# Optimization experiments

Measured on AMD Instinct MI355X. Metric: run time of the kernel, lower is better.

Reference implementation:

```python
import jax, jax.numpy as jnp
import numpy as np

RPN_BATCH = 256
ROI_BATCH = 128
IMG = 800.0


def _box_iou(a, b):
    # a: [N,4], b: [G,4] -> [N,G]
    lt = jnp.maximum(a[:, None, :2], b[None, :, :2])
    rb = jnp.minimum(a[:, None, 2:], b[None, :, 2:])
    wh = jnp.clip(rb - lt, 0.0)
    inter = wh[..., 0] * wh[..., 1]
    area_a = (a[:, 2] - a[:, 0]) * (a[:, 3] - a[:, 1])
    area_b = (b[:, 2] - b[:, 0]) * (b[:, 3] - b[:, 1])
    return inter / (area_a[:, None] + area_b[None, :] - inter + 1e-6)


def _encode(a, t):
    wa = a[:, 2] - a[:, 0]
    ha = a[:, 3] - a[:, 1]
    xa = a[:, 0] + 0.5 * wa
    ya = a[:, 1] + 0.5 * ha
    wt = t[:, 2] - t[:, 0]
    ht = t[:, 3] - t[:, 1]
    xt = t[:, 0] + 0.5 * wt
    yt = t[:, 1] + 0.5 * ht
    return jnp.stack(((xt - xa) / wa, (yt - ya) / ha,
                      jnp.log(wt / wa + 1e-6), jnp.log(ht / ha + 1e-6)), axis=1)


def _smooth_l1(x):
    ax = jnp.abs(x)
    return jnp.where(ax < 1.0, 0.5 * x * x, ax - 0.5)


def _rpn_loss_one(scores, deltas, anchors, gt):
    # scores [N,1], deltas [N,4], anchors [N,4], gt [G,4]
    ious = _box_iou(anchors, gt)                 # [N,G]
    max_iou = ious.max(axis=1)
    argmax = ious.argmax(axis=1)
    labels = jnp.full((anchors.shape[0],), -1.0, dtype=scores.dtype)
    labels = jnp.where(max_iou < 0.3, 0.0, labels)
    labels = jnp.where(max_iou > 0.7, 1.0, labels)
    labels = labels.at[jnp.argmax(ious, axis=0)].set(1.0)  # each gt's best anchor is positive
    # deterministic subsampling: keep first K in index order (replaces randperm)
    num_pos = RPN_BATCH // 2
    pos = labels == 1.0
    labels = jnp.where(pos & (jnp.cumsum(pos) > num_pos), -1.0, labels)
    n_pos = jnp.sum(labels == 1.0)
    neg = labels == 0.0
    labels = jnp.where(neg & (jnp.cumsum(neg) > (RPN_BATCH - n_pos)), -1.0, labels)
    mask = (labels != -1.0).astype(scores.dtype)
    logit = scores[:, 0]
    t = jnp.clip(labels, 0.0, 1.0)
    bce = jnp.maximum(logit, 0.0) - logit * t + jnp.log1p(jnp.exp(-jnp.abs(logit)))
    cls = jnp.sum(bce * mask) / jnp.maximum(jnp.sum(mask), 1.0)
    tgt = _encode(anchors, gt[argmax])
    posm = (labels == 1.0).astype(scores.dtype)
    n_posf = jnp.sum(posm)
    reg = jnp.where(n_posf > 0,
                    jnp.sum(_smooth_l1(deltas - tgt) * posm[:, None])
                    / jnp.maximum(n_posf * 4.0, 1.0),
                    0.0)
    return cls + reg


def _det_loss_one(cls_scores, bbox_deltas, proposals, gt, gt_labels):
    # cls_scores [P,C], bbox_deltas [P,4C], proposals [P,4], gt [G,4], gt_labels [G]
    P = proposals.shape[0]
    ious = _box_iou(proposals, gt)
    max_iou = ious.max(axis=1)
    argmax = ious.argmax(axis=1)
    assigned = jnp.where(max_iou >= 0.5, gt_labels[argmax], 0)
    num_pos = ROI_BATCH // 4
    pos = assigned > 0
    pos_rank = jnp.cumsum(pos) - 1
    neg_rank = jnp.cumsum(~pos) - 1
    idx = jnp.arange(P)
    # sort key: first up-to-num_pos positives (index order), then negatives,
    # excess positives pushed to the end -> first ROI_BATCH entries are the sample
    key = jnp.where(pos,
                    jnp.where(pos_rank < num_pos, pos_rank, 2 * P + idx),
                    P + neg_rank)
    sampled = jnp.argsort(key)[:ROI_BATCH]
    t_labels = assigned[sampled]
    matched = gt[argmax[sampled]]
    t_deltas = _encode(proposals[sampled], matched)
    logp = jax.nn.log_softmax(cls_scores[sampled], axis=-1)
    cls = -jnp.mean(jnp.take_along_axis(logp, t_labels[:, None], axis=1)[:, 0])
    pd = bbox_deltas[sampled].reshape(ROI_BATCH, -1, 4)
    preds = pd[jnp.arange(ROI_BATCH), t_labels]  # class-specific deltas
    posm = (t_labels > 0).astype(cls_scores.dtype)
    n_pos = jnp.sum(posm)
    reg = jnp.where(n_pos > 0,
                    jnp.sum(_smooth_l1(preds - t_deltas) * posm[:, None])
                    / jnp.maximum(n_pos * 4.0, 1.0),
                    0.0)
    return cls + reg


def _rand_boxes(k, prefix):
    k1, k2 = jax.random.split(k)
    xy = jax.random.uniform(k1, prefix + (2,)) * (IMG - 130.0)
    wh = jax.random.uniform(k2, prefix + (2,)) * 120.0 + 8.0
    return jnp.concatenate([xy, xy + wh], axis=-1)


def setup_inputs() -> dict:
    B, N, P, G, C = 4, 250000, 1000, 32, 81
    key = jax.random.key(0)
    ks = jax.random.split(key, 8)
    return {
        "rpn_scores": jax.random.normal(ks[0], (B, N, 1), dtype=jnp.float32),
        "rpn_deltas": jax.random.normal(ks[1], (B, N, 4), dtype=jnp.float32) * 0.1,
        "cls_scores": jax.random.normal(ks[2], (B * P, C), dtype=jnp.float32),
        "bbox_deltas": jax.random.normal(ks[3], (B * P, 4 * C), dtype=jnp.float32) * 0.1,
        "anchors": _rand_boxes(ks[4], (N,)),
        "proposals": _rand_boxes(ks[5], (B, P)),
        "gt_boxes": _rand_boxes(ks[6], (B, G)),
        "gt_labels": jax.random.randint(ks[7], (B, G), 1, C, dtype=jnp.int32),
    }


def reference(rpn_scores, rpn_deltas, cls_scores, bbox_deltas,
              anchors, proposals, gt_boxes, gt_labels):
    B, P, _ = proposals.shape
    C = cls_scores.shape[-1]
    cls_b = cls_scores.reshape(B, P, C)
    del_b = bbox_deltas.reshape(B, P, 4 * C)
    rpn = jax.vmap(lambda s, d, g: _rpn_loss_one(s, d, anchors, g))(
        rpn_scores, rpn_deltas, gt_boxes)
    det = jax.vmap(_det_loss_one)(cls_b, del_b, proposals, gt_boxes, gt_labels)
    return jnp.sum(rpn) + jnp.sum(det)
```

## Files before the change

### kernel.cpp

```cpp
#include <hip/hip_runtime.h>
#include <math.h>
#include <stdint.h>

#define B_ 4
#define N_ 250000
#define P_ 1000
#define G_ 32
#define C_ 81
#define RPN_BATCH 256
#define ROI_BATCH 128

#define ABLK 1024
#define NBA ((N_ + ABLK - 1) / ABLK)

__device__ __forceinline__ float iou_one(float a0, float a1, float a2, float a3,
                                         float areaA,
                                         float b0, float b1, float b2, float b3) {
    float ltx = fmaxf(a0, b0), lty = fmaxf(a1, b1);
    float rbx = fminf(a2, b2), rby = fminf(a3, b3);
    float w = fmaxf(rbx - ltx, 0.f), h = fmaxf(rby - lty, 0.f);
    float inter = w * h;
    float areaB = (b2 - b0) * (b3 - b1);
    return inter / (areaA + areaB - inter + 1e-6f);
}

__device__ __forceinline__ unsigned long long shfl_xor_u64(unsigned long long v, int m) {
    unsigned lo = (unsigned)v, hi = (unsigned)(v >> 32);
    lo = __shfl_xor(lo, m);
    hi = __shfl_xor(hi, m);
    return ((unsigned long long)hi << 32) | lo;
}

__device__ __forceinline__ float smooth_l1(float x) {
    float ax = fabsf(x);
    return (ax < 1.f) ? 0.5f * x * x : ax - 0.5f;
}

__global__ void __launch_bounds__(256, 6) rpn_assign(
        const float* __restrict__ anchors, const float* __restrict__ gt_boxes,
        int8_t* __restrict__ labels, int* __restrict__ posCnt, int* __restrict__ negCnt,
        unsigned long long* __restrict__ blockBest,
        float* __restrict__ sums, float* __restrict__ out, int out_size) {
    __shared__ float4 sA[ABLK];
    __shared__ unsigned char sPart[4][ABLK];
    __shared__ int sCnt[8];

    int b = blockIdx.y, tid = threadIdx.x;
    int base = blockIdx.x * ABLK;

    if (blockIdx.x == 0 && b == 0) {
        if (tid < 8) sums[tid] = 0.f;
        for (int i = tid; i < out_size; i += 256) out[i] = 0.f;
    }

    for (int t = tid; t < ABLK; t += 256) {
        int ai = base + t;
        float4 v = make_float4(0.f, 0.f, 0.f, 0.f);
        if (ai < N_) v = ((const float4*)anchors)[ai];
        sA[t] = v;
    }
    __syncthreads();

    int lane = tid & 63, wave = tid >> 6;
    int waveu = __builtin_amdgcn_readfirstlane(wave);

    const float4* gt4 = (const float4*)gt_boxes + b * G_ + waveu * 8;
    float g0[8], g1[8], g2[8], g3[8], gae[8];
#pragma unroll
    for (int j = 0; j < 8; ++j) {
        float4 g = gt4[j];
        g0[j] = g.x; g1[j] = g.y; g2[j] = g.z; g3[j] = g.w;
        gae[j] = (g.z - g.x) * (g.w - g.y) + 1e-6f;
    }

    float bi[8], bd[8]; int bx[8];
#pragma unroll
    for (int j = 0; j < 8; ++j) { bi[j] = 0.f; bd[j] = 1.f; bx[j] = 0; }

    for (int k = 0; k < ABLK / 64; ++k) {
        int a = k * 64 + lane;
        float4 A = sA[a];
        float areaA = (A.z - A.x) * (A.w - A.y);
        int gidx = base + a;
        float acc03 = 1e30f, acc07 = 1e30f;
#pragma unroll
        for (int j = 0; j < 8; ++j) {
            float ltx = fmaxf(A.x, g0[j]), lty = fmaxf(A.y, g1[j]);
            float rbx = fminf(A.z, g2[j]), rby = fminf(A.w, g3[j]);
            float w = fmaxf(rbx - ltx, 0.f), h = fmaxf(rby - lty, 0.f);
            float inter = w * h;
            float d = (areaA + gae[j]) - inter;
            acc03 = fminf(acc03, fmaf(0.3f, d, -inter));
            acc07 = fminf(acc07, fmaf(0.7f, d, -inter));
            float p1 = inter * bd[j], p2 = bi[j] * d;
            if (p1 > p2) { bi[j] = inter; bd[j] = d; bx[j] = gidx; }
        }
        sPart[wave][a] = (unsigned char)(((acc07 < 0.f) ? 2 : 0) | ((acc03 > 0.f) ? 1 : 0));
    }

#pragma unroll
    for (int j = 0; j < 8; ++j) {
        float i_ = bi[j], d_ = bd[j]; int x_ = bx[j];
        for (int m = 32; m >= 1; m >>= 1) {
            float oi = __shfl_xor(i_, m), od = __shfl_xor(d_, m);
            int ox = __shfl_xor(x_, m);
            float pa = oi * d_, pb = i_ * od;
            bool take = (pa > pb) || (pa == pb && ox < x_);
            if (take) { i_ = oi; d_ = od; x_ = ox; }
        }
        if (lane == 0) {
            float iou = i_ / d_;
            unsigned long long pk =
                (((unsigned long long)__float_as_uint(iou)) << 32) |
                (unsigned)(0xFFFFFFFFu - (unsigned)x_);
            blockBest[((size_t)b * G_ + wave * 8 + j) * NBA + blockIdx.x] = pk;
        }
    }
    __syncthreads();

    unsigned u0 = ((const unsigned*)&sPart[0][0])[tid];
    unsigned u1 = ((const unsigned*)&sPart[1][0])[tid];
    unsigned u2 = ((const unsigned*)&sPart[2][0])[tid];
    unsigned u3 = ((const unsigned*)&sPart[3][0])[tid];
    unsigned andb = u0 & u1 & u2 & u3;
    unsigned orb  = u0 | u1 | u2 | u3;
    int gbase = base + tid * 4;
    unsigned outw = 0; int cp = 0, cn = 0;
#pragma unroll
    for (int j = 0; j < 4; ++j) {
        int above = (orb >> (8 * j + 1)) & 1;
        int below = (andb >> (8 * j)) & 1;
        int lab = above ? 1 : (below ? 0 : -1);
        if (gbase + j < N_) { cp += (lab == 1); cn += (lab == 0); }
        outw |= ((unsigned)(unsigned char)(char)lab) << (8 * j);
    }
    if (gbase < N_)
        ((unsigned*)labels)[(((size_t)b * N_ + base) >> 2) + tid] = outw;

    for (int m = 32; m >= 1; m >>= 1) { cp += __shfl_xor(cp, m); cn += __shfl_xor(cn, m); }
    if (lane == 0) { sCnt[wave] = cp; sCnt[4 + wave] = cn; }
    __syncthreads();
    if (tid == 0) {
        posCnt[b * NBA + blockIdx.x] = sCnt[0] + sCnt[1] + sCnt[2] + sCnt[3];
        negCnt[b * NBA + blockIdx.x] = sCnt[4] + sCnt[5] + sCnt[6] + sCnt[7];
    }
}

__global__ void __launch_bounds__(256) rpn_promote_scan(
        const unsigned long long* __restrict__ blockBest, int8_t* __restrict__ labels,
        int* __restrict__ posCnt, int* __restrict__ negCnt,
        int* __restrict__ totPos, int* __restrict__ totNeg) {
    int b = blockIdx.x, tid = threadIdx.x;
    __shared__ int sp[256], sn[256];
    __shared__ unsigned wIdx[G_];

    sp[tid] = (tid < NBA) ? posCnt[b * NBA + tid] : 0;
    sn[tid] = (tid < NBA) ? negCnt[b * NBA + tid] : 0;

    int g = tid >> 3, sub = tid & 7;
    unsigned long long v = 0;
    for (int j = sub; j < NBA; j += 8) {
        unsigned long long x = blockBest[((size_t)b * G_ + g) * NBA + j];
        if (x > v) v = x;
    }
    for (int m = 4; m >= 1; m >>= 1) {
        unsigned long long o = shfl_xor_u64(v, m);
        if (o > v) v = o;
    }
    if (sub == 0) wIdx[g] = 0xFFFFFFFFu - (unsigned)(v & 0xFFFFFFFFull);
    __syncthreads();
    if (tid < G_) {
        unsigned w = wIdx[tid];
        bool first = true;
        for (int j = 0; j < tid; ++j) if (wIdx[j] == w) first = false;
        if (first) {
            size_t li = (size_t)b * N_ + w;
            int8_t old = labels[li];
            labels[li] = 1;
            int blk = (int)(w / ABLK);
            if (old != 1) atomicAdd(&sp[blk], 1);
            if (old == 0) atomicAdd(&sn[blk], -1);
        }
    }
    __syncthreads();

    int vp = sp[tid], vn = sn[tid];
    for (int off = 1; off < 256; off <<= 1) {
        int tp = 0, tn = 0;
        if (tid >= off) { tp = sp[tid - off]; tn = sn[tid - off]; }
        __syncthreads();
        sp[tid] += tp; sn[tid] += tn;
        __syncthreads();
    }
    if (tid < NBA) {
        posCnt[b * NBA + tid] = sp[tid] - vp;
        negCnt[b * NBA + tid] = sn[tid] - vn;
    }
    if (tid == 0) { totPos[b] = sp[255]; totNeg[b] = sn[255]; }
}

__global__ void __launch_bounds__(256) rpn_sample(
        const int8_t* __restrict__ labels, const float* __restrict__ rpn_scores,
        const float* __restrict__ rpn_deltas, const float* __restrict__ anchors,
        const float* __restrict__ gt_boxes,
        const int* __restrict__ posBase, const int* __restrict__ negBase,
        const int* __restrict__ totPos, float* __restrict__ sums) {
    int b = blockIdx.y, tid = threadIdx.x;
    int base = blockIdx.x * ABLK;
    __shared__ float sg[G_ * 4];
    __shared__ int swP[4], swN[4];
    __shared__ float sred[8];
    if (tid < G_ * 4) sg[tid] = gt_boxes[b * G_ * 4 + tid];

    int gbase = base + tid * 4;
    unsigned word = 0xFFFFFFFFu;
    if (gbase < N_)
        word = ((const unsigned*)labels)[(((size_t)b * N_ + base) >> 2) + tid];
    int lab[4]; int cntP = 0, cntN = 0;
#pragma unroll
    for (int j = 0; j < 4; ++j) {
        lab[j] = (int)(char)((word >> (8 * j)) & 0xFF);
        cntP += (lab[j] == 1); cntN += (lab[j] == 0);
    }
    int lane = tid & 63, wave = tid >> 6;
    int ip = cntP, inn = cntN;
    for (int off = 1; off < 64; off <<= 1) {
        int vp = __shfl_up(ip, off), vn = __shfl_up(inn, off);
        if (lane >= off) { ip += vp; inn += vn; }
    }
    if (lane == 63) { swP[wave] = ip; swN[wave] = inn; }
    __syncthreads();
    int bP = 0, bN = 0;
    for (int w = 0; w < wave; ++w) { bP += swP[w]; bN += swN[w]; }
    int pP = posBase[b * NBA + blockIdx.x] + bP + ip - cntP;
    int pN = negBase[b * NBA + blockIdx.x] + bN + inn - cntN;

    int npos = min(totPos[b], RPN_BATCH / 2);
    int negQ = RPN_BATCH - npos;

    float bce = 0.f, regv = 0.f;
#pragma unroll
    for (int j = 0; j < 4; ++j) {
        int i = gbase + j;
        if (i >= N_) break;
        if (lab[j] == 1) {
            int r = pP++;
            if (r < RPN_BATCH / 2) {
                float l = rpn_scores[(size_t)b * N_ + i];
                bce += fmaxf(l, 0.f) - l + log1pf(expf(-fabsf(l)));
                float4 A = ((const float4*)anchors)[i];
                float areaA = (A.z - A.x) * (A.w - A.y);
                float best = -1.f; int am = 0;
                for (int g = 0; g < G_; ++g) {
                    float iou = iou_one(A.x, A.y, A.z, A.w, areaA,
                                        sg[g * 4], sg[g * 4 + 1], sg[g * 4 + 2], sg[g * 4 + 3]);
                    if (iou > best) { best = iou; am = g; }
                }
                float t0 = sg[am * 4], t1 = sg[am * 4 + 1], t2 = sg[am * 4 + 2], t3 = sg[am * 4 + 3];
                float wa = A.z - A.x, ha = A.w - A.y;
                float xa = A.x + 0.5f * wa, ya = A.y + 0.5f * ha;
                float wt = t2 - t0, ht = t3 - t1;
                float xt = t0 + 0.5f * wt, yt = t1 + 0.5f * ht;
                float4 D = ((const float4*)rpn_deltas)[(size_t)b * N_ + i];
                regv += smooth_l1(D.x - (xt - xa) / wa) + smooth_l1(D.y - (yt - ya) / ha) +
                        smooth_l1(D.z - logf(wt / wa + 1e-6f)) + smooth_l1(D.w - logf(ht / ha + 1e-6f));
            }
        } else if (lab[j] == 0) {
            int r = pN++;
            if (r < negQ) {
                float l = rpn_scores[(size_t)b * N_ + i];
                bce += fmaxf(l, 0.f) + log1pf(expf(-fabsf(l)));
            }
        }
    }
    for (int m = 32; m >= 1; m >>= 1) { bce += __shfl_xor(bce, m); regv += __shfl_xor(regv, m); }
    if (lane == 0) { sred[wave] = bce; sred[4 + wave] = regv; }
    __syncthreads();
    if (tid == 0) {
        float sb = sred[0] + sred[1] + sred[2] + sred[3];
        float sr = sred[4] + sred[5] + sred[6] + sred[7];
        if (sb != 0.f) atomicAdd(&sums[b], sb);
        if (sr != 0.f) atomicAdd(&sums[4 + b], sr);
    }
}

__global__ void __launch_bounds__(1024) det_all(
        const float* __restrict__ cls_scores, const float* __restrict__ bbox_deltas,
        const float* __restrict__ proposals, const float* __restrict__ gt_boxes,
        const int* __restrict__ gt_labels, const int* __restrict__ totPos,
        const int* __restrict__ totNeg, const float* __restrict__ sums,
        float* __restrict__ out) {
    int b = blockIdx.x, tid = threadIdx.x;
    int lane = tid & 63, wave = tid >> 6;
    __shared__ float sgt[G_ * 4];
    __shared__ int sgl[G_];
    __shared__ short sassign[P_];
    __shared__ unsigned char sargm[P_];
    __shared__ int sw[16];
    __shared__ int ssamp[ROI_BATCH];
    __shared__ float cacc[16], racc[16];
    if (tid < G_ * 4) sgt[tid] = gt_boxes[b * G_ * 4 + tid];
    if (tid < G_) sgl[tid] = gt_labels[b * G_ + tid];
    __syncthreads();

    int lab = 0;
    if (tid < P_) {
        float4 A = ((const float4*)proposals)[b * P_ + tid];
        float areaA = (A.z - A.x) * (A.w - A.y);
        float best = -1.f; int am = 0;
#pragma unroll 8
        for (int g = 0; g < G_; ++g) {
            float iou = iou_one(A.x, A.y, A.z, A.w, areaA,
                                sgt[g * 4], sgt[g * 4 + 1], sgt[g * 4 + 2], sgt[g * 4 + 3]);
            if (iou > best) { best = iou; am = g; }
        }
        lab = (best >= 0.5f) ? sgl[am] : 0;
        sassign[tid] = (short)lab;
        sargm[tid] = (unsigned char)am;
    }

    int cnt = (tid < P_ && lab > 0) ? 1 : 0;
    int inc = cnt;
    for (int off = 1; off < 64; off <<= 1) {
        int v = __shfl_up(inc, off);
        if (lane >= off) inc += v;
    }
    if (lane == 63) sw[wave] = inc;
    __syncthreads();
    int basew = 0, total = 0;
    for (int w = 0; w < 16; ++w) { if (w < wave) basew += sw[w]; total += sw[w]; }
    int prefix = basew + inc - cnt;
    int npos_kept = min(total, ROI_BATCH / 4);
    int nneg_total = P_ - total;
    if (tid < P_) {
        int slot;
        if (lab > 0)
            slot = (prefix < ROI_BATCH / 4) ? prefix
                 : npos_kept + nneg_total + (prefix - ROI_BATCH / 4);
        else
            slot = npos_kept + (tid - prefix);
        if (slot < ROI_BATCH) ssamp[slot] = tid;
    }
    int np_det = npos_kept + max(0, ROI_BATCH - npos_kept - nneg_total);
    __syncthreads();

    float clsv = 0.f, regv = 0.f;
    for (int k = 0; k < 8; ++k) {
        int r = wave * 8 + k;
        int s = ssamp[r];
        int t = sassign[s];
        const float* row = cls_scores + ((size_t)(b * P_ + s)) * C_;
        float v1 = row[lane];
        float v2 = (lane < C_ - 64) ? row[64 + lane] : -INFINITY;
        float m = fmaxf(v1, v2);
        for (int mm = 32; mm >= 1; mm >>= 1) m = fmaxf(m, __shfl_xor(m, mm));
        float se = expf(v1 - m) + ((lane < C_ - 64) ? expf(v2 - m) : 0.f);
        for (int mm = 32; mm >= 1; mm >>= 1) se += __shfl_xor(se, mm);
        if (lane == 0) {
            clsv += -(row[t] - m - logf(se));
            if (t > 0) {
                int g = sargm[s];
                float4 A = ((const float4*)proposals)[b * P_ + s];
                float t0 = sgt[g * 4], t1 = sgt[g * 4 + 1];
                float t2 = sgt[g * 4 + 2], t3 = sgt[g * 4 + 3];
                float wa = A.z - A.x, ha = A.w - A.y;
                float xa = A.x + 0.5f * wa, ya = A.y + 0.5f * ha;
                float wt = t2 - t0, ht = t3 - t1;
                float xt = t0 + 0.5f * wt, yt = t1 + 0.5f * ht;
                const float4 pd = *(const float4*)(bbox_deltas +
                        ((size_t)(b * P_ + s)) * (4 * C_) + 4 * t);
                regv += smooth_l1(pd.x - (xt - xa) / wa) + smooth_l1(pd.y - (yt - ya) / ha) +
                        smooth_l1(pd.z - logf(wt / wa + 1e-6f)) + smooth_l1(pd.w - logf(ht / ha + 1e-6f));
            }
        }
    }
    if (lane == 0) { cacc[wave] = clsv; racc[wave] = regv; }
    __syncthreads();
    if (tid == 0) {
        float cs = 0.f, rs = 0.f;
        for (int w = 0; w < 16; ++w) { cs += cacc[w]; rs += racc[w]; }
        float cls = cs / (float)ROI_BATCH;
        float reg = (np_det > 0) ? rs / fmaxf((float)np_det * 4.f, 1.f) : 0.f;
        int rnp = min(totPos[b], RPN_BATCH / 2);
        int kneg = min(totNeg[b], RPN_BATCH - rnp);
        float rcls = sums[b] / fmaxf((float)(rnp + kneg), 1.f);
        float rreg = (rnp > 0) ? sums[4 + b] / fmaxf((float)rnp * 4.f, 1.f) : 0.f;
        atomicAdd(out, cls + reg + rcls + rreg);
    }
}

extern "C" void kernel_launch(void* const* d_in, const int* in_sizes, int n_in,
                              void* d_out, int out_size, void* d_ws, size_t ws_size,
                              hipStream_t stream) {
    const float* rpn_scores  = (const float*)d_in[0];
    const float* rpn_deltas  = (const float*)d_in[1];
    const float* cls_scores  = (const float*)d_in[2];
    const float* bbox_deltas = (const float*)d_in[3];
    const float* anchors     = (const float*)d_in[4];
    const float* proposals   = (const float*)d_in[5];
    const float* gt_boxes    = (const float*)d_in[6];
    const int*   gt_labels   = (const int*)d_in[7];
    float* out = (float*)d_out;

    char* ws = (char*)d_ws;
    size_t off = 0;
    auto alloc = [&](size_t bytes) -> char* {
        size_t o = (off + 255) & ~(size_t)255;
        off = o + bytes;
        return ws + o;
    };
    int8_t* labels = (int8_t*)alloc((size_t)B_ * N_);
    unsigned long long* blockBest = (unsigned long long*)alloc((size_t)B_ * G_ * NBA * 8);
    int* posCnt = (int*)alloc((size_t)B_ * NBA * 4);
    int* negCnt = (int*)alloc((size_t)B_ * NBA * 4);
    int* totPos = (int*)alloc(B_ * 4);
    int* totNeg = (int*)alloc(B_ * 4);
    float* sums = (float*)alloc(8 * 4);

    rpn_assign<<<dim3(NBA, B_), 256, 0, stream>>>(anchors, gt_boxes, labels,
                                                  posCnt, negCnt, blockBest,
                                                  sums, out, out_size);
    rpn_promote_scan<<<B_, 256, 0, stream>>>(blockBest, labels, posCnt, negCnt,
                                             totPos, totNeg);
    rpn_sample<<<dim3(NBA, B_), 256, 0, stream>>>(labels, rpn_scores, rpn_deltas,
                                                  anchors, gt_boxes, posCnt, negCnt,
                                                  totPos, sums);
    det_all<<<B_, 1024, 0, stream>>>(cls_scores, bbox_deltas, proposals, gt_boxes,
                                     gt_labels, totPos, totNeg, sums, out);
}
```

Before: 168.1 us.

## Fuse detection loss into RPN sampling kernel with last-block finalization

Removes the separate det_all launch by adding one extra block per image to the rpn_sample grid, which computes the detection loss with 256 threads handling four proposals each. RPN normalization moves into the last-arriving sampling block per image, found through a threadfence plus atomic done counter that is reset in rpn_assign. This saves a kernel launch and its serialization. In exchange the detection block now does four times the work per thread and may become the tail. The rpn_assign occupancy hint also drops from 6 to 4.

```diff
diff --git a/kernel.cpp b/kernel.cpp
--- a/kernel.cpp
+++ b/kernel.cpp
@@ -36,11 +36,12 @@
     return (ax < 1.f) ? 0.5f * x * x : ax - 0.5f;
 }
 
-__global__ void __launch_bounds__(256, 6) rpn_assign(
+__global__ void __launch_bounds__(256, 4) rpn_assign(
         const float* __restrict__ anchors, const float* __restrict__ gt_boxes,
         int8_t* __restrict__ labels, int* __restrict__ posCnt, int* __restrict__ negCnt,
         unsigned long long* __restrict__ blockBest,
-        float* __restrict__ sums, float* __restrict__ out, int out_size) {
+        float* __restrict__ sums, unsigned* __restrict__ doneCnt,
+        float* __restrict__ out, int out_size) {
     __shared__ float4 sA[ABLK];
     __shared__ unsigned char sPart[4][ABLK];
     __shared__ int sCnt[8];
@@ -50,6 +51,7 @@
 
     if (blockIdx.x == 0 && b == 0) {
         if (tid < 8) sums[tid] = 0.f;
+        if (tid < B_) doneCnt[tid] = 0u;
         for (int i = tid; i < out_size; i += 256) out[i] = 0.f;
     }
 
@@ -199,13 +201,126 @@
     if (tid == 0) { totPos[b] = sp[255]; totNeg[b] = sn[255]; }
 }
 
-__global__ void __launch_bounds__(256) rpn_sample(
+__global__ void __launch_bounds__(256) rpn_sample_det(
         const int8_t* __restrict__ labels, const float* __restrict__ rpn_scores,
         const float* __restrict__ rpn_deltas, const float* __restrict__ anchors,
         const float* __restrict__ gt_boxes,
+        const float* __restrict__ cls_scores, const float* __restrict__ bbox_deltas,
+        const float* __restrict__ proposals, const int* __restrict__ gt_labels,
         const int* __restrict__ posBase, const int* __restrict__ negBase,
-        const int* __restrict__ totPos, float* __restrict__ sums) {
+        const int* __restrict__ totPos, const int* __restrict__ totNeg,
+        float* __restrict__ sums, unsigned* __restrict__ doneCnt,
+        float* __restrict__ out) {
     int b = blockIdx.y, tid = threadIdx.x;
+    int lane = tid & 63, wave = tid >> 6;
+
+    if (blockIdx.x == NBA) {
+        __shared__ float sgt[G_ * 4];
+        __shared__ int sgl[G_];
+        __shared__ short sassign[1024];
+        __shared__ unsigned char sargm[1024];
+        __shared__ int sw4[4];
+        __shared__ int ssamp[ROI_BATCH];
+        __shared__ float cacc[4], racc[4];
+        if (tid < G_ * 4) sgt[tid] = gt_boxes[b * G_ * 4 + tid];
+        if (tid < G_) sgl[tid] = gt_labels[b * G_ + tid];
+        __syncthreads();
+
+        for (int k = 0; k < 4; ++k) {
+            int p = tid + k * 256;
+            if (p < P_) {
+                float4 A = ((const float4*)proposals)[b * P_ + p];
+                float areaA = (A.z - A.x) * (A.w - A.y);
+                float best = -1.f; int am = 0;
+#pragma unroll 8
+                for (int g = 0; g < G_; ++g) {
+                    float iou = iou_one(A.x, A.y, A.z, A.w, areaA,
+                                        sgt[g * 4], sgt[g * 4 + 1], sgt[g * 4 + 2], sgt[g * 4 + 3]);
+                    if (iou > best) { best = iou; am = g; }
+                }
+                sassign[p] = (best >= 0.5f) ? (short)sgl[am] : (short)0;
+                sargm[p] = (unsigned char)am;
+            }
+        }
+        __syncthreads();
+
+        int c0 = tid * 4, cnt = 0;
+#pragma unroll
+        for (int k = 0; k < 4; ++k) {
+            int p = c0 + k;
+            if (p < P_ && sassign[p] > 0) cnt++;
+        }
+        int inc = cnt;
+        for (int off = 1; off < 64; off <<= 1) {
+            int v = __shfl_up(inc, off);
+            if (lane >= off) inc += v;
+        }
+        if (lane == 63) sw4[wave] = inc;
+        __syncthreads();
+        int basew = 0, total = 0;
+        for (int w = 0; w < 4; ++w) { if (w < wave) basew += sw4[w]; total += sw4[w]; }
+        int prefix = basew + inc - cnt;
+        int npos_kept = min(total, ROI_BATCH / 4);
+        int nneg_total = P_ - total;
+#pragma unroll
+        for (int k = 0; k < 4; ++k) {
+            int p = c0 + k;
+            if (p >= P_) break;
+            int slot;
+            if (sassign[p] > 0) {
+                slot = (prefix < ROI_BATCH / 4) ? prefix
+                     : npos_kept + nneg_total + (prefix - ROI_BATCH / 4);
+                prefix++;
+            } else {
+                slot = npos_kept + (p - prefix);
+            }
+            if (slot < ROI_BATCH) ssamp[slot] = p;
+        }
+        int np_det = npos_kept + max(0, ROI_BATCH - npos_kept - nneg_total);
+        __syncthreads();
+
+        float clsv = 0.f, regv = 0.f;
+        for (int k = 0; k < 32; ++k) {
+            int r = wave * 32 + k;
+            int s = ssamp[r];
+            int t = sassign[s];
+            const float* row = cls_scores + ((size_t)(b * P_ + s)) * C_;
+            float v1 = row[lane];
+            float v2 = (lane < C_ - 64) ? row[64 + lane] : -INFINITY;
+            float m = fmaxf(v1, v2);
+            for (int mm = 32; mm >= 1; mm >>= 1) m = fmaxf(m, __shfl_xor(m, mm));
+            float se = expf(v1 - m) + ((lane < C_ - 64) ? expf(v2 - m) : 0.f);
+            for (int mm = 32; mm >= 1; mm >>= 1) se += __shfl_xor(se, mm);
+            if (lane == 0) {
+                clsv += -(row[t] - m - logf(se));
+                if (t > 0) {
+                    int g = sargm[s];
+                    float4 A = ((const float4*)proposals)[b * P_ + s];
+                    float t0 = sgt[g * 4], t1 = sgt[g * 4 + 1];
+                    float t2 = sgt[g * 4 + 2], t3 = sgt[g * 4 + 3];
+                    float wa = A.z - A.x, ha = A.w - A.y;
+                    float xa = A.x + 0.5f * wa, ya = A.y + 0.5f * ha;
+                    float wt = t2 - t0, ht = t3 - t1;
+                    float xt = t0 + 0.5f * wt, yt = t1 + 0.5f * ht;
+                    const float4 pd = *(const float4*)(bbox_deltas +
+                            ((size_t)(b * P_ + s)) * (4 * C_) + 4 * t);
+                    regv += smooth_l1(pd.x - (xt - xa) / wa) + smooth_l1(pd.y - (yt - ya) / ha) +
+                            smooth_l1(pd.z - logf(wt / wa + 1e-6f)) + smooth_l1(pd.w - logf(ht / ha + 1e-6f));
+                }
+            }
+        }
+        if (lane == 0) { cacc[wave] = clsv; racc[wave] = regv; }
+        __syncthreads();
+        if (tid == 0) {
+            float cs = cacc[0] + cacc[1] + cacc[2] + cacc[3];
+            float rs = racc[0] + racc[1] + racc[2] + racc[3];
+            float cls = cs / (float)ROI_BATCH;
+            float reg = (np_det > 0) ? rs / fmaxf((float)np_det * 4.f, 1.f) : 0.f;
+            atomicAdd(out, cls + reg);
+        }
+        return;
+    }
+
     int base = blockIdx.x * ABLK;
     __shared__ float sg[G_ * 4];
     __shared__ int swP[4], swN[4];
@@ -222,7 +337,6 @@
         lab[j] = (int)(char)((word >> (8 * j)) & 0xFF);
         cntP += (lab[j] == 1); cntN += (lab[j] == 0);
     }
-    int lane = tid & 63, wave = tid >> 6;
     int ip = cntP, inn = cntN;
     for (int off = 1; off < 64; off <<= 1) {
         int vp = __shfl_up(ip, off), vn = __shfl_up(inn, off);
@@ -281,111 +395,17 @@
         float sr = sred[4] + sred[5] + sred[6] + sred[7];
         if (sb != 0.f) atomicAdd(&sums[b], sb);
         if (sr != 0.f) atomicAdd(&sums[4 + b], sr);
-    }
-}
-
-__global__ void __launch_bounds__(1024) det_all(
-        const float* __restrict__ cls_scores, const float* __restrict__ bbox_deltas,
-        const float* __restrict__ proposals, const float* __restrict__ gt_boxes,
-        const int* __restrict__ gt_labels, const int* __restrict__ totPos,
-        const int* __restrict__ totNeg, const float* __restrict__ sums,
-        float* __restrict__ out) {
-    int b = blockIdx.x, tid = threadIdx.x;
-    int lane = tid & 63, wave = tid >> 6;
-    __shared__ float sgt[G_ * 4];
-    __shared__ int sgl[G_];
-    __shared__ short sassign[P_];
-    __shared__ unsigned char sargm[P_];
-    __shared__ int sw[16];
-    __shared__ int ssamp[ROI_BATCH];
-    __shared__ float cacc[16], racc[16];
-    if (tid < G_ * 4) sgt[tid] = gt_boxes[b * G_ * 4 + tid];
-    if (tid < G_) sgl[tid] = gt_labels[b * G_ + tid];
-    __syncthreads();
-
-    int lab = 0;
-    if (tid < P_) {
-        float4 A = ((const float4*)proposals)[b * P_ + tid];
-        float areaA = (A.z - A.x) * (A.w - A.y);
-        float best = -1.f; int am = 0;
-#pragma unroll 8
-        for (int g = 0; g < G_; ++g) {
-            float iou = iou_one(A.x, A.y, A.z, A.w, areaA,
-                                sgt[g * 4], sgt[g * 4 + 1], sgt[g * 4 + 2], sgt[g * 4 + 3]);
-            if (iou > best) { best = iou; am = g; }
-        }
-        lab = (best >= 0.5f) ? sgl[am] : 0;
-        sassign[tid] = (short)lab;
-        sargm[tid] = (unsigned char)am;
-    }
-
-    int cnt = (tid < P_ && lab > 0) ? 1 : 0;
-    int inc = cnt;
-    for (int off = 1; off < 64; off <<= 1) {
-        int v = __shfl_up(inc, off);
-        if (lane >= off) inc += v;
-    }
-    if (lane == 63) sw[wave] = inc;
-    __syncthreads();
-    int basew = 0, total = 0;
-    for (int w = 0; w < 16; ++w) { if (w < wave) basew += sw[w]; total += sw[w]; }
-    int prefix = basew + inc - cnt;
-    int npos_kept = min(total, ROI_BATCH / 4);
-    int nneg_total = P_ - total;
-    if (tid < P_) {
-        int slot;
-        if (lab > 0)
-            slot = (prefix < ROI_BATCH / 4) ? prefix
-                 : npos_kept + nneg_total + (prefix - ROI_BATCH / 4);
-        else
-            slot = npos_kept + (tid - prefix);
-        if (slot < ROI_BATCH) ssamp[slot] = tid;
-    }
-    int np_det = npos_kept + max(0, ROI_BATCH - npos_kept - nneg_total);
-    __syncthreads();
-
-    float clsv = 0.f, regv = 0.f;
-    for (int k = 0; k < 8; ++k) {
-        int r = wave * 8 + k;
-        int s = ssamp[r];
-        int t = sassign[s];
-        const float* row = cls_scores + ((size_t)(b * P_ + s)) * C_;
-        float v1 = row[lane];
-        float v2 = (lane < C_ - 64) ? row[64 + lane] : -INFINITY;
-        float m = fmaxf(v1, v2);
-        for (int mm = 32; mm >= 1; mm >>= 1) m = fmaxf(m, __shfl_xor(m, mm));
-        float se = expf(v1 - m) + ((lane < C_ - 64) ? expf(v2 - m) : 0.f);
-        for (int mm = 32; mm >= 1; mm >>= 1) se += __shfl_xor(se, mm);
-        if (lane == 0) {
-            clsv += -(row[t] - m - logf(se));
-            if (t > 0) {
-                int g = sargm[s];
-                float4 A = ((const float4*)proposals)[b * P_ + s];
-                float t0 = sgt[g * 4], t1 = sgt[g * 4 + 1];
-                float t2 = sgt[g * 4 + 2], t3 = sgt[g * 4 + 3];
-                float wa = A.z - A.x, ha = A.w - A.y;
-                float xa = A.x + 0.5f * wa, ya = A.y + 0.5f * ha;
-                float wt = t2 - t0, ht = t3 - t1;
-                float xt = t0 + 0.5f * wt, yt = t1 + 0.5f * ht;
-                const float4 pd = *(const float4*)(bbox_deltas +
-                        ((size_t)(b * P_ + s)) * (4 * C_) + 4 * t);
-                regv += smooth_l1(pd.x - (xt - xa) / wa) + smooth_l1(pd.y - (yt - ya) / ha) +
-                        smooth_l1(pd.z - logf(wt / wa + 1e-6f)) + smooth_l1(pd.w - logf(ht / ha + 1e-6f));
-            }
-        }
-    }
-    if (lane == 0) { cacc[wave] = clsv; racc[wave] = regv; }
-    __syncthreads();
-    if (tid == 0) {
-        float cs = 0.f, rs = 0.f;
-        for (int w = 0; w < 16; ++w) { cs += cacc[w]; rs += racc[w]; }
-        float cls = cs / (float)ROI_BATCH;
-        float reg = (np_det > 0) ? rs / fmaxf((float)np_det * 4.f, 1.f) : 0.f;
-        int rnp = min(totPos[b], RPN_BATCH / 2);
-        int kneg = min(totNeg[b], RPN_BATCH - rnp);
-        float rcls = sums[b] / fmaxf((float)(rnp + kneg), 1.f);
-        float rreg = (rnp > 0) ? sums[4 + b] / fmaxf((float)rnp * 4.f, 1.f) : 0.f;
-        atomicAdd(out, cls + reg + rcls + rreg);
+        __threadfence();
+        unsigned prev = atomicAdd(&doneCnt[b], 1u);
+        if (prev == NBA - 1) {
+            float csum = atomicAdd(&sums[b], 0.f);
+            float rsum = atomicAdd(&sums[4 + b], 0.f);
+            int rnp = min(totPos[b], RPN_BATCH / 2);
+            int kneg = min(totNeg[b], RPN_BATCH - rnp);
+            float rcls = csum / fmaxf((float)(rnp + kneg), 1.f);
+            float rreg = (rnp > 0) ? rsum / fmaxf((float)rnp * 4.f, 1.f) : 0.f;
+            atomicAdd(out, rcls + rreg);
+        }
     }
 }
 
@@ -416,15 +436,15 @@
     int* totPos = (int*)alloc(B_ * 4);
     int* totNeg = (int*)alloc(B_ * 4);
     float* sums = (float*)alloc(8 * 4);
+    unsigned* doneCnt = (unsigned*)alloc(B_ * 4);
 
     rpn_assign<<<dim3(NBA, B_), 256, 0, stream>>>(anchors, gt_boxes, labels,
                                                   posCnt, negCnt, blockBest,
-                                                  sums, out, out_size);
+                                                  sums, doneCnt, out, out_size);
     rpn_promote_scan<<<B_, 256, 0, stream>>>(blockBest, labels, posCnt, negCnt,
                                              totPos, totNeg);
-    rpn_sample<<<dim3(NBA, B_), 256, 0, stream>>>(labels, rpn_scores, rpn_deltas,
-                                                  anchors, gt_boxes, posCnt, negCnt,
-                                                  totPos, sums);
-    det_all<<<B_, 1024, 0, stream>>>(cls_scores, bbox_deltas, proposals, gt_boxes,
-                                     gt_labels, totPos, totNeg, sums, out);
-}
+    rpn_sample_det<<<dim3(NBA + 1, B_), 256, 0, stream>>>(
+        labels, rpn_scores, rpn_deltas, anchors, gt_boxes,
+        cls_scores, bbox_deltas, proposals, gt_labels,
+        posCnt, negCnt, totPos, totNeg, sums, doneCnt, out);
+}
```

New measurement: 175.1 us. +4.2%, slower.
